# Kernel tuning notes

Hardware: AMD Instinct MI355X
Metric: run time of the kernel (lower is better)

Reference implementation:

```python
import jax, jax.numpy as jnp
import numpy as np

B = 64        # graphs per batch
NPG = 512     # nodes per graph (batch = repeat(arange(B), NPG))
D = 128       # hidden_dim = input_dim
L = 3         # GCN layers
K = 16        # NTN tensors
BINS = 16     # histogram bins


def _prep_edges(ei, N, dtype):
    # GCNConv normalization: add self-loops, deg on targets, sym norm
    loop = jnp.arange(N)
    src = jnp.concatenate([ei[0], loop])
    dst = jnp.concatenate([ei[1], loop])
    deg = jnp.zeros((N,), dtype).at[dst].add(1.0)
    dinv = jnp.where(deg > 0, jax.lax.rsqrt(deg), 0.0)
    norm = (dinv[src] * dinv[dst])[:, None]
    return src, dst, norm


def _encode(x, src, dst, norm, gcn_w, gcn_b, bn_g, bn_b, bn_m, bn_v):
    # eval-mode BatchNorm (running stats), dropout = identity
    for l in range(L):
        h = x @ gcn_w[l].T                     # [N, D]
        x = jnp.zeros_like(h).at[dst].add(norm * h[src]) + gcn_b[l]
        x = (x - bn_m[l]) * jax.lax.rsqrt(bn_v[l] + 1e-5) * bn_g[l] + bn_b[l]
        x = jax.nn.relu(x)
    return x


def _attention_pool(emb, ctx_w, ctx_b, att_w, att_b):
    t = jnp.tanh(emb @ ctx_w.T + ctx_b)        # [N, D]
    s = (t @ att_w + att_b).reshape(B, NPG, 1)
    e = emb.reshape(B, NPG, D)
    w = jax.nn.softmax(s, axis=1)              # per-graph softmax
    return (w * e).sum(axis=1)                 # [B, D]


def _histogram(e1, e2):
    n1 = (e1 / jnp.maximum(jnp.linalg.norm(e1, axis=-1, keepdims=True), 1e-8)).reshape(B, NPG, D)
    n2 = (e2 / jnp.maximum(jnp.linalg.norm(e2, axis=-1, keepdims=True), 1e-8)).reshape(B, NPG, D)
    sims = jnp.einsum('bnd,bmd->bnm', n1, n2)  # [B, n, n] cosine sims in [-1,1]
    bi = jnp.clip(jnp.floor((sims + 1.0) * (BINS / 2.0)), 0, BINS - 1).astype(jnp.int32)
    flat = (jnp.arange(B, dtype=jnp.int32)[:, None] * BINS + bi.reshape(B, -1)).reshape(-1)
    hist = jax.ops.segment_sum(jnp.ones(flat.shape, jnp.float32), flat,
                               num_segments=B * BINS).reshape(B, BINS)
    return hist / (hist.sum(axis=1, keepdims=True) + 1e-8)


def _ntn(g1, g2, T, tb, w1, b1, w2, b2, w3, b3):
    tp = jnp.einsum('bd,kde,be->bk', g1, T, g2) + tb   # bilinear products
    h = jax.nn.relu(tp @ w1.T + b1)
    h = jax.nn.relu(h @ w2.T + b2)
    return jax.nn.sigmoid(h @ w3.T + b3)               # [B, 1]


def _forward(x1, x2, edge_index1, edge_index2,
             gcn_w, gcn_b, bn_gamma, bn_beta, bn_mean, bn_var,
             ctx_w, ctx_b, att_w, att_b,
             ntn_T, ntn_bias, ntn_w1, ntn_b1, ntn_w2, ntn_b2, ntn_w3, ntn_b3,
             hist_w1, hist_b1, hist_w2, hist_b2,
             fus_w1, fus_b1, fus_w2, fus_b2):
    N = x1.shape[0]
    s1, d1, n1 = _prep_edges(edge_index1, N, x1.dtype)
    s2, d2, n2 = _prep_edges(edge_index2, N, x2.dtype)
    e1 = _encode(x1, s1, d1, n1, gcn_w, gcn_b, bn_gamma, bn_beta, bn_mean, bn_var)
    e2 = _encode(x2, s2, d2, n2, gcn_w, gcn_b, bn_gamma, bn_beta, bn_mean, bn_var)
    g1 = _attention_pool(e1, ctx_w, ctx_b, att_w, att_b)
    g2 = _attention_pool(e2, ctx_w, ctx_b, att_w, att_b)
    ntn_sim = _ntn(g1, g2, ntn_T, ntn_bias, ntn_w1, ntn_b1, ntn_w2, ntn_b2, ntn_w3, ntn_b3)
    hist = _histogram(e1, e2)
    hemb = jax.nn.relu(hist @ hist_w1.T + hist_b1) @ hist_w2.T + hist_b2
    comb = jnp.concatenate([ntn_sim, hemb], axis=1)    # [B, 17]
    h = jax.nn.relu(comb @ fus_w1.T + fus_b1)
    return jax.nn.sigmoid(h @ fus_w2.T + fus_b2)       # [B, 1]


def setup_inputs() -> dict:
    key = jax.random.key(0)
    ks = jax.random.split(key, 32)
    N = B * NPG
    E = 16 * N
    sc = 0.05
    inp = {
        'x1': jax.random.normal(ks[0], (N, D), jnp.float32),
        'x2': jax.random.normal(ks[1], (N, D), jnp.float32),
        'edge_index1': jax.random.randint(ks[2], (2, E), 0, N),
        'edge_index2': jax.random.randint(ks[3], (2, E), 0, N),
        'batch1': jnp.repeat(jnp.arange(B), NPG),
        'batch2': jnp.repeat(jnp.arange(B), NPG),
        'gcn_w': jax.random.normal(ks[4], (L, D, D), jnp.float32) * sc,
        'gcn_b': jax.random.normal(ks[5], (L, D), jnp.float32) * sc,
        'bn_gamma': jnp.ones((L, D), jnp.float32),
        'bn_beta': jnp.zeros((L, D), jnp.float32),
        'bn_mean': jnp.zeros((L, D), jnp.float32),
        'bn_var': jnp.ones((L, D), jnp.float32),
        'ctx_w': jax.random.normal(ks[6], (D, D), jnp.float32) * sc,
        'ctx_b': jax.random.normal(ks[7], (D,), jnp.float32) * sc,
        'att_w': jax.random.normal(ks[8], (D,), jnp.float32) * sc,
        'att_b': jax.random.normal(ks[9], (1,), jnp.float32) * sc,
        'ntn_T': jax.random.normal(ks[10], (K, D, D), jnp.float32) * 0.02,
        'ntn_bias': jax.random.normal(ks[11], (K,), jnp.float32) * sc,
        'ntn_w1': jax.random.normal(ks[12], (32, K), jnp.float32) * 0.2,
        'ntn_b1': jax.random.normal(ks[13], (32,), jnp.float32) * sc,
        'ntn_w2': jax.random.normal(ks[14], (16, 32), jnp.float32) * 0.15,
        'ntn_b2': jax.random.normal(ks[15], (16,), jnp.float32) * sc,
        'ntn_w3': jax.random.normal(ks[16], (1, 16), jnp.float32) * 0.2,
        'ntn_b3': jax.random.normal(ks[17], (1,), jnp.float32) * sc,
        'hist_w1': jax.random.normal(ks[18], (32, BINS), jnp.float32) * 0.2,
        'hist_b1': jax.random.normal(ks[19], (32,), jnp.float32) * sc,
        'hist_w2': jax.random.normal(ks[20], (16, 32), jnp.float32) * 0.15,
        'hist_b2': jax.random.normal(ks[21], (16,), jnp.float32) * sc,
        'fus_w1': jax.random.normal(ks[22], (8, 17), jnp.float32) * 0.2,
        'fus_b1': jax.random.normal(ks[23], (8,), jnp.float32) * sc,
        'fus_w2': jax.random.normal(ks[24], (1, 8), jnp.float32) * 0.3,
        'fus_b2': jax.random.normal(ks[25], (1,), jnp.float32) * sc,
    }
    return inp


def reference(x1, x2, edge_index1, edge_index2, batch1, batch2,
              gcn_w, gcn_b, bn_gamma, bn_beta, bn_mean, bn_var,
              ctx_w, ctx_b, att_w, att_b,
              ntn_T, ntn_bias, ntn_w1, ntn_b1, ntn_w2, ntn_b2, ntn_w3, ntn_b3,
              hist_w1, hist_b1, hist_w2, hist_b2,
              fus_w1, fus_b1, fus_w2, fus_b2):
    # batch1/batch2 encode 64 equal-sized graphs (repeat(arange(B), NPG));
    # the per-graph loops of the torch code become dense [B, NPG, D] ops.
    return _forward(x1, x2, edge_index1, edge_index2,
                    gcn_w, gcn_b, bn_gamma, bn_beta, bn_mean, bn_var,
                    ctx_w, ctx_b, att_w, att_b,
                    ntn_T, ntn_bias, ntn_w1, ntn_b1, ntn_w2, ntn_b2, ntn_w3, ntn_b3,
                    hist_w1, hist_b1, hist_w2, hist_b2,
                    fus_w1, fus_b1, fus_w2, fus_b2)
```

## Files before the change

kernel.cpp:

```cpp
#include <hip/hip_runtime.h>
#include <math.h>

#define NN 32768
#define BB 64
#define NPG 512
#define DD 128
#define LL 3
#define EE 524288
#define NBINS 16
#define KNTN 16
#define NND (NN*DD)
#define NBKT 128
#define BCAP 10240

typedef unsigned short ushort_t;
typedef __attribute__((ext_vector_type(8))) short short8;
typedef __attribute__((ext_vector_type(4))) float f32x4;

__device__ __forceinline__ ushort_t f2bf(float f) {
    unsigned u = __builtin_bit_cast(unsigned, f);
    u += 0x7FFFu + ((u >> 16) & 1u);
    return (ushort_t)(u >> 16);
}
__device__ __forceinline__ float bf2f(ushort_t h) {
    unsigned u = ((unsigned)h) << 16;
    return __builtin_bit_cast(float, u);
}
__device__ __forceinline__ unsigned pack2(float a, float b) {
    return (unsigned)f2bf(a) | ((unsigned)f2bf(b) << 16);
}
__device__ __forceinline__ float lo16(unsigned u) { return __builtin_bit_cast(float, u << 16); }
__device__ __forceinline__ float hi16(unsigned u) { return __builtin_bit_cast(float, u & 0xffff0000u); }

__global__ __launch_bounds__(256) void k_prep(const float* __restrict__ x1,
                                              const float* __restrict__ x2,
                                              const float* __restrict__ gw,
                                              const float* __restrict__ cw,
                                              const float* __restrict__ gcn_b,
                                              const float* __restrict__ bn_g,
                                              const float* __restrict__ bn_b,
                                              const float* __restrict__ bn_m,
                                              const float* __restrict__ bn_v,
                                              ushort_t* __restrict__ Xbf,
                                              ushort_t* __restrict__ wbf,
                                              float* __restrict__ bnsc,
                                              float* __restrict__ bnsh,
                                              int* __restrict__ bcur,
                                              float* __restrict__ hist) {
    int b = blockIdx.x, t = threadIdx.x;
    if (b < 8192) {
        int i = b * 256 + t;
        const float4 v = (i < NND / 4) ? ((const float4*)x1)[i] : ((const float4*)x2)[i - NND / 4];
        uint2 o;
        o.x = pack2(v.x, v.y);
        o.y = pack2(v.z, v.w);
        ((uint2*)Xbf)[i] = o;
    } else if (b < 8256) {
        int i = (b - 8192) * 256 + t;
        const float4 v = (i < 3 * DD * DD / 4) ? ((const float4*)gw)[i]
                                               : ((const float4*)cw)[i - 3 * DD * DD / 4];
        uint2 o;
        o.x = pack2(v.x, v.y);
        o.y = pack2(v.z, v.w);
        ((uint2*)wbf)[i] = o;
    } else {
        if (t < NBKT) bcur[t] = 0;
        for (int i = t; i < BB * NBINS; i += 256) hist[i] = 0.f;
        if (t < DD) {
            #pragma unroll
            for (int l = 0; l < LL; l++) {
                int c = l * DD + t;
                float sc = bn_g[c] * rsqrtf(bn_v[c] + 1e-5f);
                bnsc[c] = sc;
                bnsh[c] = (gcn_b[c] - bn_m[c]) * sc + bn_b[c];
            }
        }
    }
}

__global__ __launch_bounds__(256) void k_bucket(const int* __restrict__ ei1,
                                                const int* __restrict__ ei2,
                                                int* __restrict__ bcur,
                                                unsigned* __restrict__ ibuf) {
    __shared__ int cnt[NBKT], off[NBKT], gb[NBKT];
    __shared__ unsigned stage[2048];
    int t = threadIdx.x;
    int blk = blockIdx.x;
    const int* ei = (blk < 256) ? ei1 : ei2;
    int ebase = (blk & 255) * 2048;
    int addn = (blk < 256) ? 0 : NN;
    for (int i = t; i < NBKT; i += 256) cnt[i] = 0;
    __syncthreads();
    unsigned pk[8]; int rk[8];
    #pragma unroll
    for (int k = 0; k < 8; k++) {
        int e = ebase + t + k * 256;
        int s = ei[e] + addn;
        int d = ei[EE + e] + addn;
        pk[k] = (unsigned)s | ((unsigned)d << 16);
    }
    #pragma unroll
    for (int k = 0; k < 8; k++) {
        int bk = pk[k] >> 25;
        rk[k] = atomicAdd(&cnt[bk], 1);
    }
    __syncthreads();
    if (t < NBKT) off[t] = cnt[t];
    __syncthreads();
    for (int o = 1; o < NBKT; o <<= 1) {
        int v = 0;
        if (t < NBKT && t >= o) v = off[t - o];
        __syncthreads();
        if (t < NBKT) off[t] += v;
        __syncthreads();
    }
    #pragma unroll
    for (int k = 0; k < 8; k++) {
        int bk = pk[k] >> 25;
        stage[off[bk] - cnt[bk] + rk[k]] = pk[k];
    }
    if (t < NBKT) {
        int c = cnt[t];
        gb[t] = c > 0 ? atomicAdd(&bcur[t], c) : 0;
    }
    __syncthreads();
    #pragma unroll
    for (int k = 0; k < 8; k++) {
        int idx = t + k * 256;
        unsigned p = stage[idx];
        int bk = p >> 25;
        int pos = idx - (off[bk] - cnt[bk]);
        ibuf[(size_t)bk * BCAP + gb[bk] + pos] = p;
    }
}

__global__ __launch_bounds__(256) void k_bcsr(const unsigned* __restrict__ ibuf,
                                              const int* __restrict__ bcur,
                                              int* __restrict__ deg,
                                              float* __restrict__ dinv,
                                              int* __restrict__ rowstart,
                                              ushort_t* __restrict__ esrc) {
    __shared__ int cnt[512];
    __shared__ int ps[256];
    __shared__ int lcur[512];
    int bk = blockIdx.x, t = threadIdx.x;
    for (int i = t; i < 512; i += 256) cnt[i] = 0;
    __syncthreads();
    int n = bcur[bk];
    const unsigned* buf = ibuf + (size_t)bk * BCAP;
    for (int i = t; i < n; i += 256) {
        int dl = (buf[i] >> 16) & 511;
        atomicAdd(&cnt[dl], 1);
    }
    __syncthreads();
    int c0 = cnt[2 * t], c1 = cnt[2 * t + 1];
    ps[t] = c0 + c1;
    __syncthreads();
    for (int o = 1; o < 256; o <<= 1) {
        int v = (t >= o) ? ps[t - o] : 0;
        __syncthreads();
        ps[t] += v;
        __syncthreads();
    }
    int excl = (t == 0) ? 0 : ps[t - 1];
    int base = bk * BCAP;
    int g0 = bk * 512 + 2 * t, g1 = g0 + 1;
    deg[g0] = c0; deg[g1] = c1;
    dinv[g0] = rsqrtf((float)c0 + 1.0f);
    dinv[g1] = rsqrtf((float)c1 + 1.0f);
    int r0 = base + excl, r1 = base + excl + c0;
    rowstart[g0] = r0;
    rowstart[g1] = r1;
    lcur[2 * t] = r0;
    lcur[2 * t + 1] = r1;
    __syncthreads();
    for (int i = t; i < n; i += 256) {
        unsigned p = buf[i];
        int dl = (p >> 16) & 511;
        int slot = atomicAdd(&lcur[dl], 1);
        esrc[slot] = (ushort_t)(p & 0xffffu);
    }
}

template<int EPI>
__global__ __launch_bounds__(256) void k_mgemm(const ushort_t* __restrict__ X,
                                               const ushort_t* __restrict__ Wb,
                                               const float* __restrict__ bias,
                                               ushort_t* __restrict__ Out,
                                               const float* __restrict__ aw,
                                               const float* __restrict__ ab,
                                               float* __restrict__ Sout,
                                               const float* __restrict__ dscale) {
    __shared__ __align__(16) ushort_t wlds[128 * 128];
    int t = threadIdx.x;
    {
        int r = t >> 1, h = t & 1;
        const uint4* src = (const uint4*)(Wb + (size_t)r * DD + h * 64);
        #pragma unroll
        for (int i = 0; i < 8; i++) {
            int co = h * 128 + i * 16;
            int sw = co ^ ((r & 7) << 4);
            *(uint4*)&wlds[r * DD + (sw >> 1)] = src[i];
        }
    }
    __syncthreads();
    int w = t >> 6, l = t & 63;
    int rw = blockIdx.x * 128 + w * 32;
    int lr = l & 15, lg = l >> 4;
    f32x4 acc[2][8];
    #pragma unroll
    for (int g = 0; g < 2; g++)
        #pragma unroll
        for (int c = 0; c < 8; c++) acc[g][c] = (f32x4){0.f, 0.f, 0.f, 0.f};
    const ushort_t* xrow0 = X + (size_t)(rw + lr) * DD + lg * 8;
    const ushort_t* xrow1 = xrow0 + (size_t)16 * DD;
    int swl = (lr & 7) << 4;
    for (int kt = 0; kt < 4; kt++) {
        short8 a0 = *(const short8*)(xrow0 + kt * 32);
        short8 a1 = *(const short8*)(xrow1 + kt * 32);
        int colsw = (kt * 64 + lg * 16) ^ swl;
        #pragma unroll
        for (int c = 0; c < 8; c++) {
            int row = c * 16 + lr;
            short8 b = *(const short8*)&wlds[row * DD + (colsw >> 1)];
            acc[0][c] = __builtin_amdgcn_mfma_f32_16x16x32_bf16(a0, b, acc[0][c], 0, 0, 0);
            acc[1][c] = __builtin_amdgcn_mfma_f32_16x16x32_bf16(a1, b, acc[1][c], 0, 0, 0);
        }
    }
    if (EPI == 0) {
        float ds[2][4];
        #pragma unroll
        for (int g = 0; g < 2; g++)
            #pragma unroll
            for (int q = 0; q < 4; q++) ds[g][q] = dscale[rw + g * 16 + lg * 4 + q];
        #pragma unroll
        for (int g = 0; g < 2; g++)
            #pragma unroll
            for (int c = 0; c < 8; c++) {
                int col = c * 16 + lr;
                #pragma unroll
                for (int q = 0; q < 4; q++)
                    Out[(size_t)(rw + g * 16 + lg * 4 + q) * DD + col] = f2bf(acc[g][c][q] * ds[g][q]);
            }
    } else {
        float rs[2][4] = {};
        #pragma unroll
        for (int c = 0; c < 8; c++) {
            int col = c * 16 + lr;
            float bv = bias[col], wv = aw[col];
            #pragma unroll
            for (int g = 0; g < 2; g++)
                #pragma unroll
                for (int q = 0; q < 4; q++)
                    rs[g][q] += tanhf(acc[g][c][q] + bv) * wv;
        }
        #pragma unroll
        for (int m = 1; m < 16; m <<= 1)
            #pragma unroll
            for (int g = 0; g < 2; g++)
                #pragma unroll
                for (int q = 0; q < 4; q++) rs[g][q] += __shfl_xor(rs[g][q], m);
        if (lr == 0) {
            float a0 = ab[0];
            #pragma unroll
            for (int g = 0; g < 2; g++)
                #pragma unroll
                for (int q = 0; q < 4; q++)
                    Sout[rw + g * 16 + lg * 4 + q] = rs[g][q] + a0;
        }
    }
}

#define GATHER(u, s) uint4 u = Hu4[(size_t)(s) * 16 + cl]
#define ACCUM(u) \
    a0 += lo16(u.x); a1 += hi16(u.x); a2 += lo16(u.y); a3 += hi16(u.y); \
    a4 += lo16(u.z); a5 += hi16(u.z); a6 += lo16(u.w); a7 += hi16(u.w)

template<int LAST>
__global__ __launch_bounds__(256) void k_agg(
    const ushort_t* __restrict__ Hs, const int* __restrict__ rowstart,
    const int* __restrict__ deg, const ushort_t* __restrict__ esrc,
    const float* __restrict__ dinv, const float* __restrict__ bnsc,
    const float* __restrict__ bnsh, ushort_t* __restrict__ A,
    ushort_t* __restrict__ Nrm) {
    int wid = (blockIdx.x * blockDim.x + threadIdx.x) >> 6;
    int l = threadIdx.x & 63;
    int q = l >> 4, cl = l & 15;
    int n = wid * 4 + q;
    const uint4* Hu4 = (const uint4*)Hs;
    int beg = rowstart[n];
    int end = beg + deg[n];
    float di = dinv[n];
    uint4 h = Hu4[(size_t)n * 16 + cl];
    float a0 = lo16(h.x), a1 = hi16(h.x), a2 = lo16(h.y), a3 = hi16(h.y);
    float a4 = lo16(h.z), a5 = hi16(h.z), a6 = lo16(h.w), a7 = hi16(h.w);
    int j = beg;
    for (; j + 8 <= end; j += 8) {
        unsigned s0 = esrc[j + 0], s1 = esrc[j + 1], s2 = esrc[j + 2], s3 = esrc[j + 3];
        unsigned s4 = esrc[j + 4], s5 = esrc[j + 5], s6 = esrc[j + 6], s7 = esrc[j + 7];
        GATHER(u0, s0); GATHER(u1, s1); GATHER(u2, s2); GATHER(u3, s3);
        GATHER(u4, s4); GATHER(u5, s5); GATHER(u6, s6); GATHER(u7, s7);
        ACCUM(u0); ACCUM(u1); ACCUM(u2); ACCUM(u3);
        ACCUM(u4); ACCUM(u5); ACCUM(u6); ACCUM(u7);
    }
    for (; j + 2 <= end; j += 2) {
        unsigned s0 = esrc[j], s1 = esrc[j + 1];
        GATHER(u0, s0); GATHER(u1, s1);
        ACCUM(u0); ACCUM(u1);
    }
    if (j < end) {
        unsigned s0 = esrc[j];
        GATHER(u0, s0);
        ACCUM(u0);
    }
    int c = cl * 8;
    float4 scA = *(const float4*)&bnsc[c], scB = *(const float4*)&bnsc[c + 4];
    float4 shA = *(const float4*)&bnsh[c], shB = *(const float4*)&bnsh[c + 4];
    float o0 = fmaf(a0 * di, scA.x, shA.x);
    float o1 = fmaf(a1 * di, scA.y, shA.y);
    float o2 = fmaf(a2 * di, scA.z, shA.z);
    float o3 = fmaf(a3 * di, scA.w, shA.w);
    float o4 = fmaf(a4 * di, scB.x, shB.x);
    float o5 = fmaf(a5 * di, scB.y, shB.y);
    float o6 = fmaf(a6 * di, scB.z, shB.z);
    float o7 = fmaf(a7 * di, scB.w, shB.w);
    uint4 av;
    av.x = pack2(fmaxf(o0, 0.f), fmaxf(o1, 0.f));
    av.y = pack2(fmaxf(o2, 0.f), fmaxf(o3, 0.f));
    av.z = pack2(fmaxf(o4, 0.f), fmaxf(o5, 0.f));
    av.w = pack2(fmaxf(o6, 0.f), fmaxf(o7, 0.f));
    ((uint4*)A)[(size_t)n * 16 + cl] = av;
    if (LAST) {
        float r0 = lo16(av.x), r1 = hi16(av.x), r2 = lo16(av.y), r3 = hi16(av.y);
        float r4 = lo16(av.z), r5 = hi16(av.z), r6 = lo16(av.w), r7 = hi16(av.w);
        float ss = ((r0 * r0 + r1 * r1) + (r2 * r2 + r3 * r3)) +
                   ((r4 * r4 + r5 * r5) + (r6 * r6 + r7 * r7));
        #pragma unroll
        for (int o = 8; o > 0; o >>= 1) ss += __shfl_xor(ss, o);
        float inv = 1.0f / fmaxf(sqrtf(ss), 1e-8f);
        uint4 nv;
        nv.x = pack2(r0 * inv, r1 * inv);
        nv.y = pack2(r2 * inv, r3 * inv);
        nv.z = pack2(r4 * inv, r5 * inv);
        nv.w = pack2(r6 * inv, r7 * inv);
        ((uint4*)Nrm)[(size_t)n * 16 + cl] = nv;
    }
}

__global__ __launch_bounds__(512) void k_pool2(const float* __restrict__ S,
                                               const ushort_t* __restrict__ Emb,
                                               float* __restrict__ G) {
    int b = blockIdx.x, t = threadIdx.x;
    __shared__ float red[512];
    __shared__ float w[512];
    __shared__ float red0[512], red1[512];
    float s = S[b * NPG + t];
    red[t] = s;
    __syncthreads();
    for (int o = 256; o > 0; o >>= 1) { if (t < o) red[t] = fmaxf(red[t], red[t + o]); __syncthreads(); }
    float m = red[0];
    __syncthreads();
    float e = expf(s - m);
    w[t] = e;
    red[t] = e;
    __syncthreads();
    for (int o = 256; o > 0; o >>= 1) { if (t < o) red[t] += red[t + o]; __syncthreads(); }
    float inv = 1.0f / red[0];
    int l = t & 63, ch = t >> 6;
    int nbase = b * NPG + ch * 64;
    float a0 = 0.f, a1 = 0.f;
    #pragma unroll 4
    for (int i = 0; i < 64; i++) {
        float wv = w[ch * 64 + i];
        unsigned u = ((const unsigned*)(Emb + (size_t)(nbase + i) * DD))[l];
        a0 += wv * lo16(u);
        a1 += wv * hi16(u);
    }
    red0[t] = a0; red1[t] = a1;
    __syncthreads();
    if (t < 64) {
        float s0 = 0.f, s1 = 0.f;
        #pragma unroll
        for (int c = 0; c < 8; c++) { s0 += red0[t + c * 64]; s1 += red1[t + c * 64]; }
        G[b * DD + 2 * t] = s0 * inv;
        G[b * DD + 2 * t + 1] = s1 * inv;
    }
}

__global__ __launch_bounds__(256) void k_hist(const ushort_t* __restrict__ N1,
                                              const ushort_t* __restrict__ N2,
                                              float* __restrict__ Hist) {
    __shared__ __align__(16) ushort_t blds[128 * 128];
    __shared__ int hl[256 * 17];
    __shared__ float hred[NBINS];
    int t = threadIdx.x, w = t >> 6, l = t & 63;
    int lr = l & 15, lg = l >> 4;
    int g = blockIdx.x >> 4, ti = (blockIdx.x >> 2) & 3, tj = blockIdx.x & 3;
    {
        int r = t >> 1, h = t & 1;
        const uint4* src = (const uint4*)(N2 + ((size_t)g * NPG + tj * 128 + r) * DD + h * 64);
        #pragma unroll
        for (int i = 0; i < 8; i++) {
            int co = h * 128 + i * 16;
            int sw = co ^ ((r & 7) << 4);
            *(uint4*)&blds[r * DD + (sw >> 1)] = src[i];
        }
    }
    #pragma unroll
    for (int i = t; i < 256 * 17; i += 256) hl[i] = 0;
    if (t < NBINS) hred[t] = 0.f;
    __syncthreads();

    const ushort_t* arow = N1 + ((size_t)g * NPG + ti * 128 + w * 32 + lr) * DD + lg * 8;
    f32x4 acc[2][8];
    #pragma unroll
    for (int r = 0; r < 2; r++)
        #pragma unroll
        for (int c = 0; c < 8; c++) acc[r][c] = (f32x4){0.f, 0.f, 0.f, 0.f};
    int swl = (lr & 7) << 4;
    for (int kt = 0; kt < 4; kt++) {
        short8 a0 = *(const short8*)(arow + kt * 32);
        short8 a1 = *(const short8*)(arow + (size_t)16 * DD + kt * 32);
        int colsw = (kt * 64 + lg * 16) ^ swl;
        #pragma unroll
        for (int c = 0; c < 8; c++) {
            int row = c * 16 + lr;
            short8 b = *(const short8*)&blds[row * DD + (colsw >> 1)];
            acc[0][c] = __builtin_amdgcn_mfma_f32_16x16x32_bf16(a0, b, acc[0][c], 0, 0, 0);
            acc[1][c] = __builtin_amdgcn_mfma_f32_16x16x32_bf16(a1, b, acc[1][c], 0, 0, 0);
        }
    }
    int base = t * 17;
    #pragma unroll
    for (int r = 0; r < 2; r++)
        #pragma unroll
        for (int c = 0; c < 8; c++)
            #pragma unroll
            for (int q = 0; q < 4; q++) {
                float sim = acc[r][c][q];
                float v = floorf((sim + 1.0f) * 8.0f);
                v = fminf(fmaxf(v, 0.f), 15.f);
                atomicAdd(&hl[base + (int)v], 1);
            }
    __syncthreads();
    int bin = t & 15, r0 = (t >> 4) * 16;
    int s = 0;
    #pragma unroll
    for (int r = 0; r < 16; r++) s += hl[(r0 + r) * 17 + bin];
    atomicAdd(&hred[bin], (float)s);
    __syncthreads();
    if (t < NBINS) atomicAdd(&Hist[g * NBINS + t], hred[t]);
}

__global__ __launch_bounds__(128) void k_ntn(const float* __restrict__ G1,
                                             const float* __restrict__ G2,
                                             const float* __restrict__ T,
                                             const float* __restrict__ tb,
                                             float* __restrict__ TP) {
    int b = blockIdx.x, k = blockIdx.y;
    int e = threadIdx.x;
    const float* Tk = T + (size_t)k * DD * DD;
    float g2e = G2[b * DD + e];
    float acc = 0.f;
    for (int d = 0; d < DD; d++) acc += G1[b * DD + d] * Tk[(size_t)d * DD + e];
    float val = acc * g2e;
    #pragma unroll
    for (int o = 32; o > 0; o >>= 1) val += __shfl_down(val, o);
    __shared__ float ps[2];
    if ((e & 63) == 0) ps[e >> 6] = val;
    __syncthreads();
    if (e == 0) TP[b * KNTN + k] = ps[0] + ps[1] + tb[k];
}

__global__ __launch_bounds__(256) void k_final(const float* __restrict__ TP, const float* __restrict__ Hist,
                        const float* nw1, const float* nb1, const float* nw2, const float* nb2,
                        const float* nw3, const float* nb3,
                        const float* hw1, const float* hb1, const float* hw2, const float* hb2,
                        const float* fw1, const float* fb1, const float* fw2, const float* fb2,
                        float* __restrict__ out) {
    __shared__ float sTP[BB * 16], sHist[BB * 16];
    __shared__ float snw1[512], snw2[512], shw1[512], shw2[512];
    __shared__ float snw3[16], snb1[32], snb2[16], shb1[32], shb2[16];
    __shared__ float sfw1[136], sfb1[8], sfw2[8], sscal[2];
    int t = threadIdx.x;
    for (int i = t; i < BB * 16; i += 256) { sTP[i] = TP[i]; sHist[i] = Hist[i]; }
    for (int i = t; i < 512; i += 256) {
        snw1[i] = nw1[i]; snw2[i] = nw2[i]; shw1[i] = hw1[i]; shw2[i] = hw2[i];
    }
    if (t < 136) sfw1[t] = fw1[t];
    if (t < 32) { snb1[t] = nb1[t]; shb1[t] = hb1[t]; }
    if (t < 16) { snb2[t] = nb2[t]; shb2[t] = hb2[t]; snw3[t] = nw3[t]; }
    if (t < 8) { sfb1[t] = fb1[t]; sfw2[t] = fw2[t]; }
    if (t == 0) { sscal[0] = nb3[0]; sscal[1] = fb2[0]; }
    __syncthreads();
    if (t >= BB) return;
    int b = t;
    float h1[32];
    #pragma unroll
    for (int i = 0; i < 32; i++) {
        float a = snb1[i];
        for (int k = 0; k < 16; k++) a += sTP[b * 16 + k] * snw1[i * 16 + k];
        h1[i] = fmaxf(a, 0.f);
    }
    float h2[16];
    #pragma unroll
    for (int j = 0; j < 16; j++) {
        float a = snb2[j];
        for (int i = 0; i < 32; i++) a += h1[i] * snw2[j * 32 + i];
        h2[j] = fmaxf(a, 0.f);
    }
    float nt = sscal[0];
    for (int j = 0; j < 16; j++) nt += h2[j] * snw3[j];
    nt = 1.f / (1.f + expf(-nt));
    float hh[16]; float sum = 0.f;
    for (int k = 0; k < 16; k++) { hh[k] = sHist[b * 16 + k]; sum += hh[k]; }
    float inv = 1.f / (sum + 1e-8f);
    for (int k = 0; k < 16; k++) hh[k] *= inv;
    float g1v[32];
    #pragma unroll
    for (int i = 0; i < 32; i++) {
        float a = shb1[i];
        for (int k = 0; k < 16; k++) a += hh[k] * shw1[i * 16 + k];
        g1v[i] = fmaxf(a, 0.f);
    }
    float hemb[16];
    #pragma unroll
    for (int j = 0; j < 16; j++) {
        float a = shb2[j];
        for (int i = 0; i < 32; i++) a += g1v[i] * shw2[j * 32 + i];
        hemb[j] = a;
    }
    float comb[17];
    comb[0] = nt;
    for (int j = 0; j < 16; j++) comb[1 + j] = hemb[j];
    float f1[8];
    #pragma unroll
    for (int i = 0; i < 8; i++) {
        float a = sfb1[i];
        for (int j = 0; j < 17; j++) a += comb[j] * sfw1[i * 17 + j];
        f1[i] = fmaxf(a, 0.f);
    }
    float o = sscal[1];
    for (int i = 0; i < 8; i++) o += f1[i] * sfw2[i];
    out[b] = 1.f / (1.f + expf(-o));
}

extern "C" void kernel_launch(void* const* d_in, const int* in_sizes, int n_in,
                              void* d_out, int out_size, void* d_ws, size_t ws_size,
                              hipStream_t stream) {
    const float* x1    = (const float*)d_in[0];
    const float* x2    = (const float*)d_in[1];
    const int*   ei1   = (const int*)d_in[2];
    const int*   ei2   = (const int*)d_in[3];
    const float* gcn_w = (const float*)d_in[6];
    const float* gcn_b = (const float*)d_in[7];
    const float* bn_g  = (const float*)d_in[8];
    const float* bn_b  = (const float*)d_in[9];
    const float* bn_m  = (const float*)d_in[10];
    const float* bn_v  = (const float*)d_in[11];
    const float* ctx_w = (const float*)d_in[12];
    const float* ctx_b = (const float*)d_in[13];
    const float* att_w = (const float*)d_in[14];
    const float* att_b = (const float*)d_in[15];
    const float* ntn_T = (const float*)d_in[16];
    const float* ntn_b = (const float*)d_in[17];
    const float* nw1 = (const float*)d_in[18];
    const float* nb1 = (const float*)d_in[19];
    const float* nw2 = (const float*)d_in[20];
    const float* nb2 = (const float*)d_in[21];
    const float* nw3 = (const float*)d_in[22];
    const float* nb3 = (const float*)d_in[23];
    const float* hw1 = (const float*)d_in[24];
    const float* hb1 = (const float*)d_in[25];
    const float* hw2 = (const float*)d_in[26];
    const float* hb2 = (const float*)d_in[27];
    const float* fw1 = (const float*)d_in[28];
    const float* fb1 = (const float*)d_in[29];
    const float* fw2 = (const float*)d_in[30];
    const float* fb2 = (const float*)d_in[31];
    float* out = (float*)d_out;

    ushort_t* Xbf = (ushort_t*)d_ws;
    ushort_t* Abf = Xbf + 2 * (size_t)NND;
    ushort_t* Hbf = Abf + 2 * (size_t)NND;
    ushort_t* wbf = Hbf + 2 * (size_t)NND;
    float* dinv = (float*)(wbf + 4 * DD * DD);
    float* S    = dinv + 2 * NN;
    float* G    = S + 2 * NN;
    float* hist = G + 2 * BB * DD;
    float* tp   = hist + BB * NBINS;
    float* bnsc = tp + BB * KNTN;
    float* bnsh = bnsc + LL * DD;
    int* degi  = (int*)(bnsh + LL * DD);
    int* rowst = degi + 2 * NN;
    int* bcur  = rowst + 2 * NN;
    ushort_t* esrc = (ushort_t*)(bcur + NBKT);
    unsigned* ibuf = (unsigned*)(esrc + (size_t)NBKT * BCAP);

    k_prep<<<8257, 256, 0, stream>>>(x1, x2, gcn_w, ctx_w, gcn_b, bn_g, bn_b, bn_m, bn_v,
                                     Xbf, wbf, bnsc, bnsh, bcur, hist);
    k_bucket<<<2 * EE / 2048, 256, 0, stream>>>(ei1, ei2, bcur, ibuf);
    k_bcsr<<<NBKT, 256, 0, stream>>>(ibuf, bcur, degi, dinv, rowst, esrc);

    for (int l = 0; l < LL; l++) {
        k_mgemm<0><<<2 * NN / 128, 256, 0, stream>>>(l == 0 ? Xbf : Abf,
                                                     wbf + (size_t)l * DD * DD,
                                                     nullptr, Hbf, nullptr, nullptr, nullptr, dinv);
        if (l < LL - 1)
            k_agg<0><<<2 * NN / 16, 256, 0, stream>>>(Hbf, rowst, degi, esrc, dinv,
                                                      bnsc + l * DD, bnsh + l * DD, Abf, nullptr);
        else
            k_agg<1><<<2 * NN / 16, 256, 0, stream>>>(Hbf, rowst, degi, esrc, dinv,
                                                      bnsc + l * DD, bnsh + l * DD, Abf, Xbf);
    }
    k_mgemm<2><<<2 * NN / 128, 256, 0, stream>>>(Abf, wbf + 3 * DD * DD, ctx_b,
                                                 nullptr, att_w, att_b, S, nullptr);
    k_pool2<<<2 * BB, 512, 0, stream>>>(S, Abf, G);
    k_hist<<<BB * 16, 256, 0, stream>>>(Xbf, Xbf + NND, hist);
    k_ntn<<<dim3(BB, KNTN), 128, 0, stream>>>(G, G + BB * DD, ntn_T, ntn_b, tp);
    k_final<<<1, 256, 0, stream>>>(tp, hist, nw1, nb1, nw2, nb2, nw3, nb3,
                                   hw1, hb1, hw2, hb2, fw1, fb1, fw2, fb2, out);
}
```

Baseline: 235.5 us.

## Fuse fp32-to-bf16 input conversion into first GEMM and vectorize CSR index loads

```diff
diff --git a/kernel.cpp b/kernel.cpp
--- a/kernel.cpp
+++ b/kernel.cpp
@@ -12,6 +12,7 @@
 #define NND (NN*DD)
 #define NBKT 128
 #define BCAP 10240
+#define ECAP 14336
 
 typedef unsigned short ushort_t;
 typedef __attribute__((ext_vector_type(8))) short short8;
@@ -32,31 +33,21 @@
 __device__ __forceinline__ float lo16(unsigned u) { return __builtin_bit_cast(float, u << 16); }
 __device__ __forceinline__ float hi16(unsigned u) { return __builtin_bit_cast(float, u & 0xffff0000u); }
 
-__global__ __launch_bounds__(256) void k_prep(const float* __restrict__ x1,
-                                              const float* __restrict__ x2,
-                                              const float* __restrict__ gw,
+__global__ __launch_bounds__(256) void k_prep(const float* __restrict__ gw,
                                               const float* __restrict__ cw,
                                               const float* __restrict__ gcn_b,
                                               const float* __restrict__ bn_g,
                                               const float* __restrict__ bn_b,
                                               const float* __restrict__ bn_m,
                                               const float* __restrict__ bn_v,
-                                              ushort_t* __restrict__ Xbf,
                                               ushort_t* __restrict__ wbf,
                                               float* __restrict__ bnsc,
                                               float* __restrict__ bnsh,
                                               int* __restrict__ bcur,
                                               float* __restrict__ hist) {
     int b = blockIdx.x, t = threadIdx.x;
-    if (b < 8192) {
+    if (b < 64) {
         int i = b * 256 + t;
-        const float4 v = (i < NND / 4) ? ((const float4*)x1)[i] : ((const float4*)x2)[i - NND / 4];
-        uint2 o;
-        o.x = pack2(v.x, v.y);
-        o.y = pack2(v.z, v.w);
-        ((uint2*)Xbf)[i] = o;
-    } else if (b < 8256) {
-        int i = (b - 8192) * 256 + t;
         const float4 v = (i < 3 * DD * DD / 4) ? ((const float4*)gw)[i]
                                                : ((const float4*)cw)[i - 3 * DD * DD / 4];
         uint2 o;
@@ -154,7 +145,8 @@
     }
     __syncthreads();
     int c0 = cnt[2 * t], c1 = cnt[2 * t + 1];
-    ps[t] = c0 + c1;
+    int p0 = (c0 + 7) & ~7, p1 = (c1 + 7) & ~7;
+    ps[t] = p0 + p1;
     __syncthreads();
     for (int o = 1; o < 256; o <<= 1) {
         int v = (t >= o) ? ps[t - o] : 0;
@@ -163,12 +155,12 @@
         __syncthreads();
     }
     int excl = (t == 0) ? 0 : ps[t - 1];
-    int base = bk * BCAP;
+    int base = bk * ECAP;
     int g0 = bk * 512 + 2 * t, g1 = g0 + 1;
     deg[g0] = c0; deg[g1] = c1;
     dinv[g0] = rsqrtf((float)c0 + 1.0f);
     dinv[g1] = rsqrtf((float)c1 + 1.0f);
-    int r0 = base + excl, r1 = base + excl + c0;
+    int r0 = base + excl, r1 = base + excl + p0;
     rowstart[g0] = r0;
     rowstart[g1] = r1;
     lcur[2 * t] = r0;
@@ -182,8 +174,10 @@
     }
 }
 
-template<int EPI>
+template<int EPI, int XF>
 __global__ __launch_bounds__(256) void k_mgemm(const ushort_t* __restrict__ X,
+                                               const float* __restrict__ Xf1,
+                                               const float* __restrict__ Xf2,
                                                const ushort_t* __restrict__ Wb,
                                                const float* __restrict__ bias,
                                                ushort_t* __restrict__ Out,
@@ -214,10 +208,31 @@
         for (int c = 0; c < 8; c++) acc[g][c] = (f32x4){0.f, 0.f, 0.f, 0.f};
     const ushort_t* xrow0 = X + (size_t)(rw + lr) * DD + lg * 8;
     const ushort_t* xrow1 = xrow0 + (size_t)16 * DD;
+    const float* xf0 = nullptr;
+    if (XF) {
+        const float* xb = (rw < NN) ? Xf1 : (Xf2 - (size_t)NN * DD);
+        xf0 = xb + (size_t)(rw + lr) * DD + lg * 8;
+    }
     int swl = (lr & 7) << 4;
     for (int kt = 0; kt < 4; kt++) {
-        short8 a0 = *(const short8*)(xrow0 + kt * 32);
-        short8 a1 = *(const short8*)(xrow1 + kt * 32);
+        short8 a0, a1;
+        if (XF) {
+            float4 va = *(const float4*)(xf0 + kt * 32);
+            float4 vb = *(const float4*)(xf0 + kt * 32 + 4);
+            float4 vc = *(const float4*)(xf0 + (size_t)16 * DD + kt * 32);
+            float4 vd = *(const float4*)(xf0 + (size_t)16 * DD + kt * 32 + 4);
+            a0[0] = (short)f2bf(va.x); a0[1] = (short)f2bf(va.y);
+            a0[2] = (short)f2bf(va.z); a0[3] = (short)f2bf(va.w);
+            a0[4] = (short)f2bf(vb.x); a0[5] = (short)f2bf(vb.y);
+            a0[6] = (short)f2bf(vb.z); a0[7] = (short)f2bf(vb.w);
+            a1[0] = (short)f2bf(vc.x); a1[1] = (short)f2bf(vc.y);
+            a1[2] = (short)f2bf(vc.z); a1[3] = (short)f2bf(vc.w);
+            a1[4] = (short)f2bf(vd.x); a1[5] = (short)f2bf(vd.y);
+            a1[6] = (short)f2bf(vd.z); a1[7] = (short)f2bf(vd.w);
+        } else {
+            a0 = *(const short8*)(xrow0 + kt * 32);
+            a1 = *(const short8*)(xrow1 + kt * 32);
+        }
         int colsw = (kt * 64 + lg * 16) ^ swl;
         #pragma unroll
         for (int c = 0; c < 8; c++) {
@@ -294,24 +309,26 @@
     uint4 h = Hu4[(size_t)n * 16 + cl];
     float a0 = lo16(h.x), a1 = hi16(h.x), a2 = lo16(h.y), a3 = hi16(h.y);
     float a4 = lo16(h.z), a5 = hi16(h.z), a6 = lo16(h.w), a7 = hi16(h.w);
-    int j = beg;
-    for (; j + 8 <= end; j += 8) {
-        unsigned s0 = esrc[j + 0], s1 = esrc[j + 1], s2 = esrc[j + 2], s3 = esrc[j + 3];
-        unsigned s4 = esrc[j + 4], s5 = esrc[j + 5], s6 = esrc[j + 6], s7 = esrc[j + 7];
-        GATHER(u0, s0); GATHER(u1, s1); GATHER(u2, s2); GATHER(u3, s3);
-        GATHER(u4, s4); GATHER(u5, s5); GATHER(u6, s6); GATHER(u7, s7);
-        ACCUM(u0); ACCUM(u1); ACCUM(u2); ACCUM(u3);
-        ACCUM(u4); ACCUM(u5); ACCUM(u6); ACCUM(u7);
-    }
-    for (; j + 2 <= end; j += 2) {
-        unsigned s0 = esrc[j], s1 = esrc[j + 1];
-        GATHER(u0, s0); GATHER(u1, s1);
-        ACCUM(u0); ACCUM(u1);
-    }
-    if (j < end) {
-        unsigned s0 = esrc[j];
-        GATHER(u0, s0);
-        ACCUM(u0);
+    for (int j = beg; j < end; j += 8) {
+        uint4 iv = *(const uint4*)(esrc + j);
+        unsigned s0 = iv.x & 0xffffu, s1 = iv.x >> 16;
+        unsigned s2 = iv.y & 0xffffu, s3 = iv.y >> 16;
+        unsigned s4 = iv.z & 0xffffu, s5 = iv.z >> 16;
+        unsigned s6 = iv.w & 0xffffu, s7 = iv.w >> 16;
+        if (j + 8 <= end) {
+            GATHER(u0, s0); GATHER(u1, s1); GATHER(u2, s2); GATHER(u3, s3);
+            GATHER(u4, s4); GATHER(u5, s5); GATHER(u6, s6); GATHER(u7, s7);
+            ACCUM(u0); ACCUM(u1); ACCUM(u2); ACCUM(u3);
+            ACCUM(u4); ACCUM(u5); ACCUM(u6); ACCUM(u7);
+        } else {
+            { GATHER(u0, s0); ACCUM(u0); }
+            if (j + 2 <= end) { GATHER(u1, s1); ACCUM(u1); }
+            if (j + 3 <= end) { GATHER(u2, s2); ACCUM(u2); }
+            if (j + 4 <= end) { GATHER(u3, s3); ACCUM(u3); }
+            if (j + 5 <= end) { GATHER(u4, s4); ACCUM(u4); }
+            if (j + 6 <= end) { GATHER(u5, s5); ACCUM(u5); }
+            if (j + 7 <= end) { GATHER(u6, s6); ACCUM(u6); }
+        }
     }
     int c = cl * 8;
     float4 scA = *(const float4*)&bnsc[c], scB = *(const float4*)&bnsc[c + 4];
@@ -595,17 +612,22 @@
     int* rowst = degi + 2 * NN;
     int* bcur  = rowst + 2 * NN;
     ushort_t* esrc = (ushort_t*)(bcur + NBKT);
-    unsigned* ibuf = (unsigned*)(esrc + (size_t)NBKT * BCAP);
-
-    k_prep<<<8257, 256, 0, stream>>>(x1, x2, gcn_w, ctx_w, gcn_b, bn_g, bn_b, bn_m, bn_v,
-                                     Xbf, wbf, bnsc, bnsh, bcur, hist);
+    unsigned* ibuf = (unsigned*)(esrc + (size_t)NBKT * ECAP);
+
+    k_prep<<<65, 256, 0, stream>>>(gcn_w, ctx_w, gcn_b, bn_g, bn_b, bn_m, bn_v,
+                                   wbf, bnsc, bnsh, bcur, hist);
     k_bucket<<<2 * EE / 2048, 256, 0, stream>>>(ei1, ei2, bcur, ibuf);
     k_bcsr<<<NBKT, 256, 0, stream>>>(ibuf, bcur, degi, dinv, rowst, esrc);
 
     for (int l = 0; l < LL; l++) {
-        k_mgemm<0><<<2 * NN / 128, 256, 0, stream>>>(l == 0 ? Xbf : Abf,
-                                                     wbf + (size_t)l * DD * DD,
-                                                     nullptr, Hbf, nullptr, nullptr, nullptr, dinv);
+        if (l == 0)
+            k_mgemm<0, 1><<<2 * NN / 128, 256, 0, stream>>>(nullptr, x1, x2,
+                                                            wbf, nullptr, Hbf,
+                                                            nullptr, nullptr, nullptr, dinv);
+        else
+            k_mgemm<0, 0><<<2 * NN / 128, 256, 0, stream>>>(Abf, nullptr, nullptr,
+                                                            wbf + (size_t)l * DD * DD,
+                                                            nullptr, Hbf, nullptr, nullptr, nullptr, dinv);
         if (l < LL - 1)
             k_agg<0><<<2 * NN / 16, 256, 0, stream>>>(Hbf, rowst, degi, esrc, dinv,
                                                       bnsc + l * DD, bnsh + l * DD, Abf, nullptr);
@@ -613,8 +635,9 @@
             k_agg<1><<<2 * NN / 16, 256, 0, stream>>>(Hbf, rowst, degi, esrc, dinv,
                                                       bnsc + l * DD, bnsh + l * DD, Abf, Xbf);
     }
-    k_mgemm<2><<<2 * NN / 128, 256, 0, stream>>>(Abf, wbf + 3 * DD * DD, ctx_b,
-                                                 nullptr, att_w, att_b, S, nullptr);
+    k_mgemm<2, 0><<<2 * NN / 128, 256, 0, stream>>>(Abf, nullptr, nullptr,
+                                                    wbf + 3 * DD * DD, ctx_b,
+                                                    nullptr, att_w, att_b, S, nullptr);
     k_pool2<<<2 * BB, 512, 0, stream>>>(S, Abf, G);
     k_hist<<<BB * 16, 256, 0, stream>>>(Xbf, Xbf + NND, hist);
     k_ntn<<<dim3(BB, KNTN), 128, 0, stream>>>(G, G + BB * DD, ntn_T, ntn_b, tp);
```

Result: slower. 253.7 us (+7.8%).
